# Optimization experiments

Hardware: AMD Instinct MI355X
Metric: run time of the kernel (lower is better)

## Reference

```python
import jax, jax.numpy as jnp
import numpy as np

N_ATOMS = 50000
N_EDGES = 1_600_000
H = 128
EPS = 1e-3  # keras BatchNormalization default epsilon


def _bn(x, gamma, beta, mean, var):
    # inference-mode batch norm with moving statistics
    return gamma * (x - mean) * jax.lax.rsqrt(var + EPS) + beta


def setup_inputs() -> dict:
    key = jax.random.key(0)
    ks = jax.random.split(key, 16)
    s = 0.05
    D1 = H + 1
    inp = {
        "atom_embedding": jax.random.normal(ks[0], (N_ATOMS, H), jnp.float32),
        "bond_embedding": jax.random.normal(ks[1], (N_EDGES, H), jnp.float32),
        "indices_i": jax.random.randint(ks[2], (N_EDGES,), 0, N_ATOMS, dtype=jnp.int32),
        "indices_j": jax.random.randint(ks[3], (N_EDGES,), 0, N_ATOMS, dtype=jnp.int32),
        # preprocess: Dense(3H -> H+1, no bias) + BN, Dense(H+1 -> H+1, no bias) + BN
        "W1": jax.random.normal(ks[4], (3 * H, D1), jnp.float32) * s,
        "g1": jnp.ones((D1,), jnp.float32),
        "b1": jnp.zeros((D1,), jnp.float32),
        "m1": jnp.zeros((D1,), jnp.float32),
        "v1": jnp.ones((D1,), jnp.float32),
        "W2": jax.random.normal(ks[5], (D1, D1), jnp.float32) * s,
        "g2": jnp.ones((D1,), jnp.float32),
        "b2": jnp.zeros((D1,), jnp.float32),
        "m2": jnp.zeros((D1,), jnp.float32),
        "v2": jnp.ones((D1,), jnp.float32),
        # two residual layers, each: x + (x@w1+b1)@w2+b2 (activation=None)
        "r1w1": jax.random.normal(ks[6], (H, H), jnp.float32) * s,
        "r1b1": jnp.zeros((H,), jnp.float32),
        "r1w2": jax.random.normal(ks[7], (H, H), jnp.float32) * s,
        "r1b2": jnp.zeros((H,), jnp.float32),
        "r2w1": jax.random.normal(ks[8], (H, H), jnp.float32) * s,
        "r2b1": jnp.zeros((H,), jnp.float32),
        "r2w2": jax.random.normal(ks[9], (H, H), jnp.float32) * s,
        "r2b2": jnp.zeros((H,), jnp.float32),
    }
    return inp


def reference(atom_embedding, bond_embedding, indices_i, indices_j,
              W1, g1, b1, m1, v1, W2, g2, b2, m2, v2,
              r1w1, r1b1, r1w2, r1b2, r2w1, r2b1, r2w2, r2b2):
    # gather endpoints: [E, H]
    ai = atom_embedding[indices_i]
    aj = atom_embedding[indices_j]
    x = jnp.concatenate([ai, bond_embedding, aj], axis=-1)  # [E, 3H]
    x = _bn(x @ W1, g1, b1, m1, v1)  # [E, H+1]
    x = _bn(x @ W2, g2, b2, m2, v2)  # [E, H+1]
    msg = x[:, :1] * x[:, 1:]  # gate * message -> [E, H]
    atom = atom_embedding + jax.ops.segment_sum(msg, indices_i, num_segments=N_ATOMS)
    # residual MLPs (activation=None -> identity)
    atom = atom + (atom @ r1w1 + r1b1) @ r1w2 + r1b2
    atom = atom + (atom @ r2w1 + r2b1) @ r2w2 + r2b2
    return atom
```

## Files before the change

### kernel.cpp

```cpp
#include <hip/hip_runtime.h>

#define NA 50000
#define NE 1600000
#define HH 128
#define D1 129
#define EPS 1e-3f

typedef __bf16 bf16_t;
typedef bf16_t bf16x8 __attribute__((ext_vector_type(8)));
typedef bf16_t bf16x4 __attribute__((ext_vector_type(4)));
typedef float f32x4 __attribute__((ext_vector_type(4)));

#define OFF_A1   0
#define OFF_C1   129
#define OFF_A2   258
#define OFF_C2   387
#define OFF_WEFF 516
#define OFF_DVEC (OFF_WEFF + 384*129)
#define OFF_Q1   (OFF_DVEC + 129)
#define OFF_Q2   (OFF_Q1 + 128*128)
#define OFF_q1   (OFF_Q2 + 128*128)
#define OFF_q2   (OFF_q1 + 128)
#define OFF_QF   (OFF_q2 + 128)
#define OFF_qf   (OFF_QF + 128*128)
#define OFF_WMT  (((OFF_qf + 128) + 3) & ~3)
#define OFF_WTT  (OFF_WMT + 9216)
#define OFF_WBT  (OFF_WTT + 9216)
#define OFF_QFT  (OFF_WBT + 9216)
#define OFF_PI   (OFF_QFT + 8192)
#define OFF_PJ   (OFF_PI + NA*D1)
#define OFF_ACC  (OFF_PJ + NA*D1)
#define OFF_ACC2 (OFF_ACC + NA*HH)
#define OFF_CNT  (OFF_ACC2 + NA)
#define OFF_CUR  (OFF_CNT + NA)
#define OFF_EDG  (OFF_CUR + NA)
#define OFF_PART (OFF_EDG + NE)
#define OFF_IIS  (OFF_PART + 256)
#define OFF_JJS  (OFF_IIS + NE)
#define SCAN_NB  ((NA + 255) / 256)

__global__ void k_affine(const float* __restrict__ g1, const float* __restrict__ b1,
                         const float* __restrict__ m1, const float* __restrict__ v1,
                         const float* __restrict__ g2, const float* __restrict__ b2,
                         const float* __restrict__ m2, const float* __restrict__ v2,
                         float* __restrict__ ws) {
    for (int idx = threadIdx.x; idx < 2 * D1; idx += blockDim.x) {
        if (idx < D1) {
            float a = g1[idx] * rsqrtf(v1[idx] + EPS);
            ws[OFF_A1 + idx] = a;
            ws[OFF_C1 + idx] = b1[idx] - m1[idx] * a;
        } else {
            int n = idx - D1;
            float a = g2[n] * rsqrtf(v2[n] + EPS);
            ws[OFF_A2 + n] = a;
            ws[OFF_C2 + n] = b2[n] - m2[n] * a;
        }
    }
}

__global__ void k_weff(const float* __restrict__ W1, const float* __restrict__ W2,
                       float* __restrict__ ws) {
    int idx = blockIdx.x * blockDim.x + threadIdx.x;
    if (idx >= 384 * D1 + D1) return;
    const float* a1 = ws + OFF_A1;
    const float* c1 = ws + OFF_C1;
    const float* a2 = ws + OFF_A2;
    const float* c2 = ws + OFF_C2;
    if (idx < 384 * D1) {
        int k = idx / D1, n = idx % D1;
        float s = 0.f;
        for (int t = 0; t < D1; ++t)
            s += W1[(size_t)k * D1 + t] * a1[t] * W2[(size_t)t * D1 + n];
        ws[OFF_WEFF + idx] = s * a2[n];
    } else {
        int n = idx - 384 * D1;
        float s = 0.f;
        for (int t = 0; t < D1; ++t)
            s += c1[t] * W2[(size_t)t * D1 + n];
        ws[OFF_DVEC + n] = s * a2[n] + c2[n];
    }
}

__global__ void k_resid(const float* __restrict__ r1w1, const float* __restrict__ r1b1,
                        const float* __restrict__ r1w2, const float* __restrict__ r1b2,
                        const float* __restrict__ r2w1, const float* __restrict__ r2b1,
                        const float* __restrict__ r2w2, const float* __restrict__ r2b2,
                        float* __restrict__ ws) {
    int idx = blockIdx.x * blockDim.x + threadIdx.x;
    if (idx >= 2 * (128 * 128 + 128)) return;
    int layer = idx / (128 * 128 + 128);
    int r = idx % (128 * 128 + 128);
    const float* w1 = layer ? r2w1 : r1w1;
    const float* b1 = layer ? r2b1 : r1b1;
    const float* w2 = layer ? r2w2 : r1w2;
    const float* b2 = layer ? r2b2 : r1b2;
    float* Q = ws + (layer ? OFF_Q2 : OFF_Q1);
    float* q = ws + (layer ? OFF_q2 : OFF_q1);
    if (r < 128 * 128) {
        int i = r >> 7, j = r & 127;
        float s = (i == j) ? 1.f : 0.f;
        for (int t = 0; t < 128; ++t)
            s += w1[i * 128 + t] * w2[t * 128 + j];
        Q[r] = s;
    } else {
        int j = r - 128 * 128;
        float s = b2[j];
        for (int t = 0; t < 128; ++t)
            s += b1[t] * w2[t * 128 + j];
        q[j] = s;
    }
}

__global__ void k_qf(float* __restrict__ ws) {
    int idx = blockIdx.x * blockDim.x + threadIdx.x;
    if (idx >= 128 * 128 + 128) return;
    const float* Q1 = ws + OFF_Q1;
    const float* Q2 = ws + OFF_Q2;
    if (idx < 128 * 128) {
        int i = idx >> 7, j = idx & 127;
        float s = 0.f;
        for (int m = 0; m < 128; ++m)
            s += Q1[i * 128 + m] * Q2[m * 128 + j];
        ws[OFF_QF + idx] = s;
    } else {
        int j = idx - 128 * 128;
        const float* q1 = ws + OFF_q1;
        float s = ws[OFF_q2 + j];
        for (int m = 0; m < 128; ++m)
            s += q1[m] * Q2[m * 128 + j];
        ws[OFF_qf + j] = s;
    }
}

__global__ void k_pack(float* __restrict__ ws) {
    int idx = blockIdx.x * blockDim.x + threadIdx.x;
    const float* Weff = ws + OFF_WEFF;
    if (idx < 18432) {
        int n = idx >> 7, k = idx & 127;
        float v = (n < 128) ? Weff[(size_t)(128 + k) * D1 + n + 1]
                            : ((n == 128) ? Weff[(size_t)(128 + k) * D1] : 0.f);
        ((bf16_t*)(ws + OFF_WMT))[idx] = (bf16_t)v;
    } else if (idx < 2 * 18432) {
        int r = idx - 18432;
        int n = r >> 7, k = r & 127;
        float v = (n < D1) ? Weff[(size_t)k * D1 + n] : 0.f;
        ((bf16_t*)(ws + OFF_WTT))[r] = (bf16_t)v;
    } else if (idx < 3 * 18432) {
        int r = idx - 2 * 18432;
        int n = r >> 7, k = r & 127;
        float v = (n < D1) ? Weff[(size_t)(256 + k) * D1 + n] : 0.f;
        ((bf16_t*)(ws + OFF_WBT))[r] = (bf16_t)v;
    } else if (idx < 3 * 18432 + 16384) {
        int r = idx - 3 * 18432;
        int n = r >> 7, k = r & 127;
        ((bf16_t*)(ws + OFF_QFT))[r] = (bf16_t)ws[OFF_QF + k * 128 + n];
    }
}

__global__ void k_hist(const int* __restrict__ idx_i, float* __restrict__ ws) {
    int e = blockIdx.x * blockDim.x + threadIdx.x;
    if (e < NE) atomicAdd((int*)(ws + OFF_CNT) + idx_i[e], 1);
}

__global__ void k_scan1(float* __restrict__ ws) {
    const int* cnt = (const int*)(ws + OFF_CNT);
    int i = blockIdx.x * 256 + threadIdx.x;
    int v = (i < NA) ? cnt[i] : 0;
#pragma unroll
    for (int o = 1; o < 64; o <<= 1) v += __shfl_xor(v, o);
    __shared__ int wsum[4];
    if ((threadIdx.x & 63) == 0) wsum[threadIdx.x >> 6] = v;
    __syncthreads();
    if (threadIdx.x == 0)
        ((int*)(ws + OFF_PART))[blockIdx.x] = wsum[0] + wsum[1] + wsum[2] + wsum[3];
}

__global__ void k_scan2(float* __restrict__ ws) {
    int* part = (int*)(ws + OFF_PART);
    __shared__ int ps[256];
    int t = threadIdx.x;
    int v = (t < SCAN_NB) ? part[t] : 0;
    ps[t] = v;
    __syncthreads();
    for (int o = 1; o < 256; o <<= 1) {
        int u = (t >= o) ? ps[t - o] : 0;
        __syncthreads();
        ps[t] += u;
        __syncthreads();
    }
    part[t] = t ? ps[t - 1] : 0;
}

__global__ void k_scan3(float* __restrict__ ws) {
    const int* cnt = (const int*)(ws + OFF_CNT);
    int* cursor = (int*)(ws + OFF_CUR);
    int base = ((const int*)(ws + OFF_PART))[blockIdx.x];
    int i = blockIdx.x * 256 + threadIdx.x;
    int v = (i < NA) ? cnt[i] : 0;
    int lane = threadIdx.x & 63, w = threadIdx.x >> 6;
    int s = v;
#pragma unroll
    for (int o = 1; o < 64; o <<= 1) {
        int u = __shfl_up(s, o);
        if (lane >= o) s += u;
    }
    __shared__ int wtot[4];
    if (lane == 63) wtot[w] = s;
    __syncthreads();
    int add = 0;
    for (int k = 0; k < 4; ++k)
        if (k < w) add += wtot[k];
    if (i < NA) cursor[i] = base + add + s - v;
}

__global__ void k_scatter(const int* __restrict__ idx_i, const int* __restrict__ idx_j,
                          float* __restrict__ ws) {
    int e = blockIdx.x * blockDim.x + threadIdx.x;
    if (e < NE) {
        int i = idx_i[e];
        int p = atomicAdd((int*)(ws + OFF_CUR) + i, 1);
        ((int*)(ws + OFF_EDG))[p] = e;
        ((int*)(ws + OFF_IIS))[p] = i;
        ((int*)(ws + OFF_JJS))[p] = idx_j[e];
    }
}

__global__ __launch_bounds__(256) void k_gemm_mfma(
    const float* __restrict__ A, const float* __restrict__ A2,
    const float* __restrict__ Pi, const float* __restrict__ acc2,
    const bf16_t* __restrict__ Wt, const float* __restrict__ bias,
    float* __restrict__ C, int ldc, int N, int ntiles, int M) {
    __shared__ __align__(16) bf16_t As[64][136];
    int t = threadIdx.x;
    int m0 = blockIdx.x * 64;
#pragma unroll
    for (int it = 0; it < 8; ++it) {
        int idx = t + 256 * it;
        int r = idx >> 5, c4 = idx & 31;
        int grow = m0 + r;
        float4 v = make_float4(0.f, 0.f, 0.f, 0.f);
        if (grow < M) {
            v = ((const float4*)(A + (size_t)grow * 128))[c4];
            if (A2) {
                float4 w = ((const float4*)(A2 + (size_t)grow * 128))[c4];
                v.x += w.x; v.y += w.y; v.z += w.z; v.w += w.w;
            }
            if (acc2) {
                float s = acc2[grow];
                const float* p = Pi + (size_t)grow * D1 + 1 + c4 * 4;
                v.x += s * p[0]; v.y += s * p[1]; v.z += s * p[2]; v.w += s * p[3];
            }
        }
        bf16x4 tmp;
        tmp[0] = (bf16_t)v.x; tmp[1] = (bf16_t)v.y; tmp[2] = (bf16_t)v.z; tmp[3] = (bf16_t)v.w;
        *(bf16x4*)&As[r][c4 * 4] = tmp;
    }
    __syncthreads();
    int lane = t & 63, w = t >> 6;
    int ll = lane & 15, quad = lane >> 4;
    bf16x8 a[4];
#pragma unroll
    for (int k = 0; k < 4; ++k)
        a[k] = *(const bf16x8*)&As[w * 16 + ll][k * 32 + quad * 8];
    for (int nt = 0; nt < ntiles; ++nt) {
        const bf16_t* bp = Wt + (size_t)(nt * 16 + ll) * 128 + quad * 8;
        f32x4 acc = {0.f, 0.f, 0.f, 0.f};
#pragma unroll
        for (int k = 0; k < 4; ++k) {
            bf16x8 b = *(const bf16x8*)(bp + k * 32);
            acc = __builtin_amdgcn_mfma_f32_16x16x32_bf16(a[k], b, acc, 0, 0, 0);
        }
        int col = nt * 16 + ll;
        if (col < N) {
            float bv = bias ? bias[col] : 0.f;
#pragma unroll
            for (int r = 0; r < 4; ++r) {
                int row = m0 + w * 16 + quad * 4 + r;
                if (row < M) C[(size_t)row * ldc + col] = acc[r] + bv;
            }
        }
    }
}

__global__ __launch_bounds__(256) void k_pipj(
    const float* __restrict__ A, const bf16_t* __restrict__ Wt,
    const float* __restrict__ bias, float* __restrict__ Ct,
    const bf16_t* __restrict__ Wb, float* __restrict__ Cb, int M) {
    __shared__ __align__(16) bf16_t As[64][136];
    int t = threadIdx.x;
    int m0 = blockIdx.x * 64;
#pragma unroll
    for (int it = 0; it < 8; ++it) {
        int idx = t + 256 * it;
        int r = idx >> 5, c4 = idx & 31;
        int grow = m0 + r;
        float4 v = make_float4(0.f, 0.f, 0.f, 0.f);
        if (grow < M) v = ((const float4*)(A + (size_t)grow * 128))[c4];
        bf16x4 tmp;
        tmp[0] = (bf16_t)v.x; tmp[1] = (bf16_t)v.y; tmp[2] = (bf16_t)v.z; tmp[3] = (bf16_t)v.w;
        *(bf16x4*)&As[r][c4 * 4] = tmp;
    }
    __syncthreads();
    int lane = t & 63, w = t >> 6;
    int ll = lane & 15, quad = lane >> 4;
    bf16x8 a[4];
#pragma unroll
    for (int k = 0; k < 4; ++k)
        a[k] = *(const bf16x8*)&As[w * 16 + ll][k * 32 + quad * 8];
    for (int half = 0; half < 2; ++half) {
        const bf16_t* W = half ? Wb : Wt;
        float* C = half ? Cb : Ct;
        for (int nt = 0; nt < 9; ++nt) {
            const bf16_t* bp = W + (size_t)(nt * 16 + ll) * 128 + quad * 8;
            f32x4 acc = {0.f, 0.f, 0.f, 0.f};
#pragma unroll
            for (int k = 0; k < 4; ++k) {
                bf16x8 b = *(const bf16x8*)(bp + k * 32);
                acc = __builtin_amdgcn_mfma_f32_16x16x32_bf16(a[k], b, acc, 0, 0, 0);
            }
            int col = nt * 16 + ll;
            if (col < D1) {
                float bv = (half == 0 && bias) ? bias[col] : 0.f;
#pragma unroll
                for (int r = 0; r < 4; ++r) {
                    int row = m0 + w * 16 + quad * 4 + r;
                    if (row < M) C[(size_t)row * D1 + col] = acc[r] + bv;
                }
            }
        }
    }
}

__global__ __launch_bounds__(256, 3) void k_edge_mfma(
    const float* __restrict__ bond, const int* __restrict__ edge_of,
    const int* __restrict__ ii_srt, const int* __restrict__ jj_srt,
    const bf16_t* __restrict__ WmidT,
    const float* __restrict__ Pi, const float* __restrict__ Pj,
    float* __restrict__ accb, float* __restrict__ acc2) {
    __shared__ __align__(16) bf16_t As[2][64][136];
    __shared__ int ii2[2][64], jj2[2][64];

    int t = threadIdx.x;
    int lane = t & 63, w = t >> 6;
    int ll = lane & 15, quad = lane >> 4;
    size_t p0 = (size_t)blockIdx.x * 256;

    bf16x8 bg[4], bn0[4], bn1[4];
    {
        const bf16_t* gp = WmidT + (size_t)(128 + ll) * 128 + quad * 8;
        const bf16_t* q0 = WmidT + (size_t)(w * 32 + ll) * 128 + quad * 8;
        const bf16_t* q1 = WmidT + (size_t)(w * 32 + 16 + ll) * 128 + quad * 8;
#pragma unroll
        for (int k = 0; k < 4; ++k) {
            bg[k] = *(const bf16x8*)(gp + k * 32);
            bn0[k] = *(const bf16x8*)(q0 + k * 32);
            bn1[k] = *(const bf16x8*)(q1 + k * 32);
        }
    }
    int n0 = w * 32 + ll, n1 = w * 32 + 16 + ll;

#pragma unroll
    for (int it = 0; it < 8; ++it) {
        int idx = t + 256 * it;
        int r = idx >> 5, c4 = idx & 31;
        int e = edge_of[p0 + r];
        float4 v = ((const float4*)(bond + (size_t)e * 128))[c4];
        bf16x4 tmp;
        tmp[0] = (bf16_t)v.x; tmp[1] = (bf16_t)v.y; tmp[2] = (bf16_t)v.z; tmp[3] = (bf16_t)v.w;
        *(bf16x4*)&As[0][r][c4 * 4] = tmp;
    }
    if (t < 64) {
        ii2[0][t] = ii_srt[p0 + t];
        jj2[0][t] = jj_srt[p0 + t];
    }
    __syncthreads();

    for (int tt = 0; tt < 4; ++tt) {
        int buf = tt & 1;

        float4 pf[8];
        int ni = 0, nj = 0;
        if (tt < 3) {
            size_t nb = p0 + (size_t)(tt + 1) * 64;
#pragma unroll
            for (int it = 0; it < 8; ++it) {
                int idx = t + 256 * it;
                int r = idx >> 5, c4 = idx & 31;
                int e = edge_of[nb + r];
                pf[it] = ((const float4*)(bond + (size_t)e * 128))[c4];
            }
            if (t < 64) {
                ni = ii_srt[nb + t];
                nj = jj_srt[nb + t];
            }
        }

#pragma unroll
        for (int g = 0; g < 4; ++g) {
            int eb = g * 16;
            bf16x8 a[4];
#pragma unroll
            for (int k = 0; k < 4; ++k)
                a[k] = *(const bf16x8*)&As[buf][eb + ll][k * 32 + quad * 8];

            int my = ii2[buf][eb + ll];
            int pv = ll ? ii2[buf][eb + ll - 1] : my;
            unsigned bmask = (unsigned)(__ballot(lane < 16 && my != pv) & 0xFFFFull);

            f32x4 ag = {0.f, 0.f, 0.f, 0.f};
#pragma unroll
            for (int k = 0; k < 4; ++k)
                ag = __builtin_amdgcn_mfma_f32_16x16x32_bf16(a[k], bg[k], ag, 0, 0, 0);
            float gl[4];
#pragma unroll
            for (int r = 0; r < 4; ++r) {
                float v = ag[r];
                if (ll == 0) {
                    int ie = ii2[buf][eb + quad * 4 + r];
                    int je = jj2[buf][eb + quad * 4 + r];
                    v += Pi[(size_t)ie * D1] + Pj[(size_t)je * D1];
                }
                gl[r] = __shfl(v, lane & 48);
            }

            if (w == 0) {
                int rs = 0;
                while (rs < 16) {
                    unsigned rest = bmask >> (rs + 1);
                    int re = rest ? rs + 1 + __builtin_ctz(rest) : 16;
                    float s = 0.f;
#pragma unroll
                    for (int r = 0; r < 4; ++r) {
                        int ee = quad * 4 + r;
                        if (ee >= rs && ee < re) s += gl[r];
                    }
                    s += __shfl_xor(s, 16);
                    s += __shfl_xor(s, 32);
                    if (lane == 0) atomicAdd(&acc2[ii2[buf][eb + rs]], s);
                    rs = re;
                }
            }

            float pj0[4], pj1[4];
#pragma unroll
            for (int r = 0; r < 4; ++r) {
                const float* pjr = Pj + (size_t)jj2[buf][eb + quad * 4 + r] * D1 + 1;
                pj0[r] = pjr[n0];
                pj1[r] = pjr[n1];
            }
            f32x4 ac0 = {0.f, 0.f, 0.f, 0.f}, ac1 = {0.f, 0.f, 0.f, 0.f};
#pragma unroll
            for (int k = 0; k < 4; ++k)
                ac0 = __builtin_amdgcn_mfma_f32_16x16x32_bf16(a[k], bn0[k], ac0, 0, 0, 0);
#pragma unroll
            for (int k = 0; k < 4; ++k)
                ac1 = __builtin_amdgcn_mfma_f32_16x16x32_bf16(a[k], bn1[k], ac1, 0, 0, 0);
            float m0[4], m1[4];
#pragma unroll
            for (int r = 0; r < 4; ++r) {
                m0[r] = gl[r] * (ac0[r] + pj0[r]);
                m1[r] = gl[r] * (ac1[r] + pj1[r]);
            }

            int rs = 0;
            while (rs < 16) {
                unsigned rest = bmask >> (rs + 1);
                int re = rest ? rs + 1 + __builtin_ctz(rest) : 16;
                float s0 = 0.f, s1 = 0.f;
#pragma unroll
                for (int r = 0; r < 4; ++r) {
                    int ee = quad * 4 + r;
                    if (ee >= rs && ee < re) { s0 += m0[r]; s1 += m1[r]; }
                }
                s0 += __shfl_xor(s0, 16);
                s0 += __shfl_xor(s0, 32);
                s1 += __shfl_xor(s1, 16);
                s1 += __shfl_xor(s1, 32);
                if (quad == 0) {
                    float* ab = accb + (size_t)ii2[buf][eb + rs] * 128;
                    atomicAdd(ab + n0, s0);
                    atomicAdd(ab + n1, s1);
                }
                rs = re;
            }
        }

        if (tt < 3) {
            int nbuf = buf ^ 1;
#pragma unroll
            for (int it = 0; it < 8; ++it) {
                int idx = t + 256 * it;
                int r = idx >> 5, c4 = idx & 31;
                bf16x4 tmp;
                tmp[0] = (bf16_t)pf[it].x; tmp[1] = (bf16_t)pf[it].y;
                tmp[2] = (bf16_t)pf[it].z; tmp[3] = (bf16_t)pf[it].w;
                *(bf16x4*)&As[nbuf][r][c4 * 4] = tmp;
            }
            if (t < 64) {
                ii2[nbuf][t] = ni;
                jj2[nbuf][t] = nj;
            }
        }
        __syncthreads();
    }
}

extern "C" void kernel_launch(void* const* d_in, const int* in_sizes, int n_in,
                              void* d_out, int out_size, void* d_ws, size_t ws_size,
                              hipStream_t stream) {
    const float* atom = (const float*)d_in[0];
    const float* bond = (const float*)d_in[1];
    const int* idx_i = (const int*)d_in[2];
    const int* idx_j = (const int*)d_in[3];
    const float* W1 = (const float*)d_in[4];
    const float* g1 = (const float*)d_in[5];
    const float* b1 = (const float*)d_in[6];
    const float* m1 = (const float*)d_in[7];
    const float* v1 = (const float*)d_in[8];
    const float* W2 = (const float*)d_in[9];
    const float* g2 = (const float*)d_in[10];
    const float* b2 = (const float*)d_in[11];
    const float* m2 = (const float*)d_in[12];
    const float* v2 = (const float*)d_in[13];
    const float* r1w1 = (const float*)d_in[14];
    const float* r1b1 = (const float*)d_in[15];
    const float* r1w2 = (const float*)d_in[16];
    const float* r1b2 = (const float*)d_in[17];
    const float* r2w1 = (const float*)d_in[18];
    const float* r2b1 = (const float*)d_in[19];
    const float* r2w2 = (const float*)d_in[20];
    const float* r2b2 = (const float*)d_in[21];
    float* ws = (float*)d_ws;
    float* out = (float*)d_out;

    hipMemsetAsync(ws + OFF_ACC, 0, (size_t)(NA * HH + 2 * NA) * sizeof(float), stream);

    k_hist<<<(NE + 255) / 256, 256, 0, stream>>>(idx_i, ws);
    k_scan1<<<SCAN_NB, 256, 0, stream>>>(ws);
    k_scan2<<<1, 256, 0, stream>>>(ws);
    k_scan3<<<SCAN_NB, 256, 0, stream>>>(ws);
    k_scatter<<<(NE + 255) / 256, 256, 0, stream>>>(idx_i, idx_j, ws);

    k_affine<<<1, 256, 0, stream>>>(g1, b1, m1, v1, g2, b2, m2, v2, ws);
    k_weff<<<(384 * D1 + D1 + 255) / 256, 256, 0, stream>>>(W1, W2, ws);
    k_resid<<<(2 * (128 * 128 + 128) + 255) / 256, 256, 0, stream>>>(
        r1w1, r1b1, r1w2, r1b2, r2w1, r2b1, r2w2, r2b2, ws);
    k_qf<<<(128 * 128 + 128 + 255) / 256, 256, 0, stream>>>(ws);
    k_pack<<<(3 * 18432 + 16384 + 255) / 256, 256, 0, stream>>>(ws);

    int gblocks = (NA + 63) / 64;
    k_pipj<<<gblocks, 256, 0, stream>>>(
        atom, (const bf16_t*)(ws + OFF_WTT), ws + OFF_DVEC, ws + OFF_PI,
        (const bf16_t*)(ws + OFF_WBT), ws + OFF_PJ, NA);

    k_edge_mfma<<<NE / 256, 256, 0, stream>>>(
        bond, (const int*)(ws + OFF_EDG), (const int*)(ws + OFF_IIS),
        (const int*)(ws + OFF_JJS), (const bf16_t*)(ws + OFF_WMT),
        ws + OFF_PI, ws + OFF_PJ, ws + OFF_ACC, ws + OFF_ACC2);

    k_gemm_mfma<<<gblocks, 256, 0, stream>>>(
        atom, ws + OFF_ACC, ws + OFF_PI, ws + OFF_ACC2, (const bf16_t*)(ws + OFF_QFT),
        ws + OFF_qf, out, 128, 128, 8, NA);
}
```

Baseline: 1.710 ms.

## Keep edge indices in registers and prefetch Pi/Pj gathers one group ahead

Removes the shared-memory index arrays ii2/jj2. Each wave now holds its 64 sorted i/j indices in registers and broadcasts them with shuffles. The Pj/Pi row gathers for the next 16-edge group, including the first group of the next tile, are issued before the current group's MFMAs so their latency overlaps compute. This raises register pressure under launch_bounds(256,3) and adds shuffle instructions.

After: 1.737 ms. About the same (+1.6%).

```diff
diff --git a/kernel.cpp b/kernel.cpp
--- a/kernel.cpp
+++ b/kernel.cpp
@@ -338,7 +338,6 @@
     const float* __restrict__ Pi, const float* __restrict__ Pj,
     float* __restrict__ accb, float* __restrict__ acc2) {
     __shared__ __align__(16) bf16_t As[2][64][136];
-    __shared__ int ii2[2][64], jj2[2][64];
 
     int t = threadIdx.x;
     int lane = t & 63, w = t >> 6;
@@ -358,6 +357,9 @@
         }
     }
     int n0 = w * 32 + ll, n1 = w * 32 + 16 + ll;
+
+    int mi = ii_srt[p0 + lane];
+    int mj = jj_srt[p0 + lane];
 
 #pragma unroll
     for (int it = 0; it < 8; ++it) {
@@ -369,17 +371,32 @@
         tmp[0] = (bf16_t)v.x; tmp[1] = (bf16_t)v.y; tmp[2] = (bf16_t)v.z; tmp[3] = (bf16_t)v.w;
         *(bf16x4*)&As[0][r][c4 * 4] = tmp;
     }
-    if (t < 64) {
-        ii2[0][t] = ii_srt[p0 + t];
-        jj2[0][t] = jj_srt[p0 + t];
-    }
     __syncthreads();
+
+    auto gather = [&](int smi, int smj, int eb2, float* p0v, float* p1v,
+                      float* piv, float* pgv) {
+#pragma unroll
+        for (int r = 0; r < 4; ++r) {
+            int jrr = __shfl(smj, eb2 + quad * 4 + r);
+            int irr = __shfl(smi, eb2 + quad * 4 + r);
+            const float* pjr = Pj + (size_t)jrr * D1;
+            p0v[r] = pjr[1 + n0];
+            p1v[r] = pjr[1 + n1];
+            if (ll == 0) {
+                piv[r] = Pi[(size_t)irr * D1];
+                pgv[r] = pjr[0];
+            }
+        }
+    };
+
+    float pj0c[4], pj1c[4], pic[4], pjgc[4];
+    gather(mi, mj, 0, pj0c, pj1c, pic, pjgc);
 
     for (int tt = 0; tt < 4; ++tt) {
         int buf = tt & 1;
 
         float4 pf[8];
-        int ni = 0, nj = 0;
+        int nmi = 0, nmj = 0;
         if (tt < 3) {
             size_t nb = p0 + (size_t)(tt + 1) * 64;
 #pragma unroll
@@ -389,10 +406,8 @@
                 int e = edge_of[nb + r];
                 pf[it] = ((const float4*)(bond + (size_t)e * 128))[c4];
             }
-            if (t < 64) {
-                ni = ii_srt[nb + t];
-                nj = jj_srt[nb + t];
-            }
+            nmi = ii_srt[nb + lane];
+            nmj = jj_srt[nb + lane];
         }
 
 #pragma unroll
@@ -403,9 +418,13 @@
             for (int k = 0; k < 4; ++k)
                 a[k] = *(const bf16x8*)&As[buf][eb + ll][k * 32 + quad * 8];
 
-            int my = ii2[buf][eb + ll];
-            int pv = ll ? ii2[buf][eb + ll - 1] : my;
-            unsigned bmask = (unsigned)(__ballot(lane < 16 && my != pv) & 0xFFFFull);
+            int my = __shfl(mi, eb + ll);
+            int pv = __shfl(mi, eb + (ll ? ll - 1 : 0));
+            unsigned bmask = (unsigned)(__ballot(lane < 16 && ll > 0 && my != pv) & 0xFFFFull);
+
+            float pj0n[4], pj1n[4], pin[4], pjgn[4];
+            if (g < 3) gather(mi, mj, eb + 16, pj0n, pj1n, pin, pjgn);
+            else if (tt < 3) gather(nmi, nmj, 0, pj0n, pj1n, pin, pjgn);
 
             f32x4 ag = {0.f, 0.f, 0.f, 0.f};
 #pragma unroll
@@ -415,11 +434,7 @@
 #pragma unroll
             for (int r = 0; r < 4; ++r) {
                 float v = ag[r];
-                if (ll == 0) {
-                    int ie = ii2[buf][eb + quad * 4 + r];
-                    int je = jj2[buf][eb + quad * 4 + r];
-                    v += Pi[(size_t)ie * D1] + Pj[(size_t)je * D1];
-                }
+                if (ll == 0) v += pic[r] + pjgc[r];
                 gl[r] = __shfl(v, lane & 48);
             }
 
@@ -436,18 +451,12 @@
                     }
                     s += __shfl_xor(s, 16);
                     s += __shfl_xor(s, 32);
-                    if (lane == 0) atomicAdd(&acc2[ii2[buf][eb + rs]], s);
+                    int irs = __shfl(mi, eb + rs);
+                    if (lane == 0) atomicAdd(&acc2[irs], s);
                     rs = re;
                 }
             }
 
-            float pj0[4], pj1[4];
-#pragma unroll
-            for (int r = 0; r < 4; ++r) {
-                const float* pjr = Pj + (size_t)jj2[buf][eb + quad * 4 + r] * D1 + 1;
-                pj0[r] = pjr[n0];
-                pj1[r] = pjr[n1];
-            }
             f32x4 ac0 = {0.f, 0.f, 0.f, 0.f}, ac1 = {0.f, 0.f, 0.f, 0.f};
 #pragma unroll
             for (int k = 0; k < 4; ++k)
@@ -458,8 +467,8 @@
             float m0[4], m1[4];
 #pragma unroll
             for (int r = 0; r < 4; ++r) {
-                m0[r] = gl[r] * (ac0[r] + pj0[r]);
-                m1[r] = gl[r] * (ac1[r] + pj1[r]);
+                m0[r] = gl[r] * (ac0[r] + pj0c[r]);
+                m1[r] = gl[r] * (ac1[r] + pj1c[r]);
             }
 
             int rs = 0;
@@ -476,12 +485,21 @@
                 s0 += __shfl_xor(s0, 32);
                 s1 += __shfl_xor(s1, 16);
                 s1 += __shfl_xor(s1, 32);
+                int irs = __shfl(mi, eb + rs);
                 if (quad == 0) {
-                    float* ab = accb + (size_t)ii2[buf][eb + rs] * 128;
+                    float* ab = accb + (size_t)irs * 128;
                     atomicAdd(ab + n0, s0);
                     atomicAdd(ab + n1, s1);
                 }
                 rs = re;
+            }
+
+            if (g < 3 || tt < 3) {
+#pragma unroll
+                for (int r = 0; r < 4; ++r) {
+                    pj0c[r] = pj0n[r]; pj1c[r] = pj1n[r];
+                    pic[r] = pin[r];   pjgc[r] = pjgn[r];
+                }
             }
         }
 
@@ -496,10 +514,8 @@
                 tmp[2] = (bf16_t)pf[it].z; tmp[3] = (bf16_t)pf[it].w;
                 *(bf16x4*)&As[nbuf][r][c4 * 4] = tmp;
             }
-            if (t < 64) {
-                ii2[nbuf][t] = ni;
-                jj2[nbuf][t] = nj;
-            }
+            mi = nmi;
+            mj = nmj;
         }
         __syncthreads();
     }
```
